# Optimization experiments

Measured on AMD Instinct MI355X. Metric: run time of the kernel, lower is better.

## Reference

```python
import jax, jax.numpy as jnp
import numpy as np

# Grid constants (from init_kwargs)
N_PIX_LO = 256
OVERSAMP = 4
N_PIX_HI = N_PIX_LO * OVERSAMP          # 1024
PIXSCALE_LO = 0.1                        # arcsec / low-res pixel
PIXSCALE_HI = PIXSCALE_LO / OVERSAMP     # arcsec / hi-res pixel
FOV_HALF_HI = 0.5 * (N_PIX_HI - 1) * PIXSCALE_HI
NV = 64
VEL0 = 0.0
DV = 10.0
M = 4_000_000                            # total cloudlet samples (N_clouds * K_vel)

# 8 trilinear corner offsets (x fastest pattern matches torch stacks)
OX = jnp.array([0, 0, 0, 0, 1, 1, 1, 1], dtype=jnp.int32)
OY = jnp.array([0, 0, 1, 1, 0, 0, 1, 1], dtype=jnp.int32)
OV = jnp.array([0, 1, 0, 1, 0, 1, 0, 1], dtype=jnp.int32)


def setup_inputs() -> dict:
    key = jax.random.key(0)
    k1, k2, k3, k4 = jax.random.split(key, 4)
    # positions mostly inside the FoV so most points survive the in-bounds mask
    ra = (jax.random.uniform(k1, (M,), dtype=jnp.float32) - 0.5) * (2.0 * FOV_HALF_HI * 0.95)
    dec = (jax.random.uniform(k2, (M,), dtype=jnp.float32) - 0.5) * (2.0 * FOV_HALF_HI * 0.95)
    vel = jax.random.uniform(k3, (M,), dtype=jnp.float32) * (DV * (NV - 2))
    flux = jax.random.uniform(k4, (M,), dtype=jnp.float32)
    return {"ra": ra, "dec": dec, "vel": vel, "flux": flux}


def _index_and_frac(x):
    i0 = jnp.floor(x)
    return i0.astype(jnp.int32), x - i0


def reference(ra, dec, vel, flux):
    # continuous hi-res grid coordinates
    ix0, fx = _index_and_frac((ra + FOV_HALF_HI) / PIXSCALE_HI)
    iy0, fy = _index_and_frac((dec + FOV_HALF_HI) / PIXSCALE_HI)
    iv0, fv = _index_and_frac((vel - VEL0) / DV)

    # in-bounds mask (instead of boolean compaction, for static shapes under jit)
    mask = ((ix0 >= 0) & (ix0 < N_PIX_HI - 1)
            & (iy0 >= 0) & (iy0 < N_PIX_HI - 1)
            & (iv0 >= 0) & (iv0 < NV - 1))

    # [M, 8] corner indices
    ix = ix0[:, None] + OX
    iy = iy0[:, None] + OY
    iv = iv0[:, None] + OV

    # [M, 8] trilinear weights: (1-f) for offset 0, f for offset 1
    wx = jnp.where(OX == 0, 1.0 - fx[:, None], fx[:, None])
    wy = jnp.where(OY == 0, 1.0 - fy[:, None], fy[:, None])
    wv = jnp.where(OV == 0, 1.0 - fv[:, None], fv[:, None])

    f_w = flux[:, None] * (wx * wy * wv) * mask[:, None].astype(flux.dtype)

    idx = (iv * N_PIX_HI + iy) * N_PIX_HI + ix          # flat voxel index [M, 8]
    idx = jnp.where(mask[:, None], idx, 0)              # out-of-bounds -> bin 0, weight 0

    cube_flat = jnp.zeros(NV * N_PIX_HI * N_PIX_HI, dtype=flux.dtype)
    cube_flat = cube_flat.at[idx.reshape(-1)].add(f_w.reshape(-1))

    # box-downsample: (Nv, H_lo, s, W_lo, s) -> mean over the two oversample axes
    cube_hi = cube_flat.reshape(NV, N_PIX_LO, OVERSAMP, N_PIX_LO, OVERSAMP)
    cube_lo = cube_hi.mean(axis=(-1, -3))               # (Nv, N_pix_lo, N_pix_lo)
    return cube_lo
```

## Files before the change

kernel.cpp:

```cpp
#include <hip/hip_runtime.h>
#include <hip/hip_fp16.h>

constexpr int   kNpixHi = 1024;
constexpr int   kNpixLo = 256;
constexpr int   kNv     = 64;
constexpr float kFov    = 12.7875f;
constexpr float kPsHi   = 0.025f;
constexpr float kDv     = 10.0f;
constexpr float kVel0   = 0.0f;

constexpr int kTileW        = 128;
constexpr int kTileH        = 64;
constexpr int kTilePix      = kTileW * kTileH;
constexpr int kBinsPerPlane = 8;
constexpr int kNumBins      = 64 * kBinsPerPlane;
constexpr int kBinCapIdeal  = 16384;
constexpr int kBinCapMin    = 13500;
constexpr int kThreadsK1    = 512;
constexpr int kWavesK1      = kThreadsK1 / 64;
constexpr int kSamplesPerBlock = 4096;
constexpr int kLdsRecCap    = 8192;
constexpr int kThreadsK2    = 1024;

typedef unsigned int u32x4 __attribute__((ext_vector_type(4)));
typedef unsigned long long u64;

__device__ __forceinline__ u64 pack_rec(unsigned idx, float w0, float w1) {
  const unsigned pk = (unsigned)__half_as_ushort(__float2half(w0))
                    | ((unsigned)__half_as_ushort(__float2half(w1)) << 16);
  return ((u64)pk << 16) | idx;
}

__device__ __forceinline__ void sys_store64(u64* p, u64 v) {
  __hip_atomic_store(p, v, __ATOMIC_RELAXED, __HIP_MEMORY_SCOPE_SYSTEM);
}

__device__ __forceinline__ __half2 h2_from_u32(unsigned pk) {
  return __builtin_bit_cast(__half2, pk);
}

enum EmitMode { kCount, kLds, kDirect };

template <EmitMode MODE>
__device__ __forceinline__ void emit(int bin, unsigned idx, float w0, float w1,
                                     unsigned int* s_cnt,
                                     const unsigned int* s_base,
                                     const unsigned int* s_ofs,
                                     u64* lds_rec,
                                     u64* __restrict__ recs,
                                     unsigned int binCap) {
  if (MODE == kCount) {
    atomicAdd(&s_cnt[bin], 1u);
    return;
  }
  const unsigned off = atomicAdd(&s_cnt[bin], 1u);
  if (MODE == kLds) {
    lds_rec[s_ofs[bin] + off] = pack_rec(idx, w0, w1);
  } else {
    const unsigned slot = s_base[bin] + off;
    if (slot < binCap)
      sys_store64(&recs[(size_t)bin * binCap + slot], pack_rec(idx, w0, w1));
  }
}

template <EmitMode MODE>
__device__ __forceinline__ void process_sample(float rr, float dd, float vv, float ff,
                                               unsigned int* s_cnt,
                                               const unsigned int* s_base,
                                               const unsigned int* s_ofs,
                                               u64* lds_rec,
                                               u64* __restrict__ recs,
                                               unsigned int binCap) {
  const float x = (rr + kFov) / kPsHi;
  const float y = (dd + kFov) / kPsHi;
  const float w = (vv - kVel0) / kDv;

  const float xf = floorf(x), yf = floorf(y), wf = floorf(w);
  const int ix0 = (int)xf, iy0 = (int)yf, iv0 = (int)wf;

  if (ix0 < 0 || ix0 >= kNpixHi - 1 ||
      iy0 < 0 || iy0 >= kNpixHi - 1 ||
      iv0 < 0 || iv0 >= kNv - 1)
    return;

  const float fx = x - xf, fy = y - yf, fv = w - wf;

  const float fw  = ff * 0.0625f;
  const float wv0 = fw * (1.0f - fv);
  const float wv1 = fw * fv;

  const int lx0 = ix0 >> 2, lx1 = (ix0 + 1) >> 2;
  const int ly0 = iy0 >> 2, ly1 = (iy0 + 1) >> 2;
  const bool tx = (lx1 != lx0), ty = (ly1 != ly0);
  const float wx0 = tx ? (1.0f - fx) : 1.0f;
  const float wy0 = ty ? (1.0f - fy) : 1.0f;

#define EMIT_PIX(lx, ly, wxy)                                                \
  {                                                                          \
    const int sb  = (((ly) >> 6) << 1) | ((lx) >> 7);                        \
    const int bin = (iv0 << 3) | sb;                                         \
    const unsigned idx = (unsigned)(((ly) & (kTileH - 1)) * kTileW +         \
                                    ((lx) & (kTileW - 1)));                  \
    emit<MODE>(bin, idx, (wxy) * wv0, (wxy) * wv1,                           \
               s_cnt, s_base, s_ofs, lds_rec, recs, binCap);                 \
  }

  EMIT_PIX(lx0, ly0, wx0 * wy0)
  if (tx)       EMIT_PIX(lx1, ly0, fx * wy0)
  if (ty)       EMIT_PIX(lx0, ly1, wx0 * fy)
  if (tx && ty) EMIT_PIX(lx1, ly1, fx * fy)
#undef EMIT_PIX
}

__global__ __launch_bounds__(kThreadsK1) void scatter_kernel(
    const float* __restrict__ ra, const float* __restrict__ dec,
    const float* __restrict__ vel, const float* __restrict__ flux,
    u64* __restrict__ recs, unsigned int* __restrict__ cursors,
    int m, unsigned int binCap) {
  __shared__ unsigned int s_cnt[kNumBins];
  __shared__ unsigned int s_base[kNumBins];
  __shared__ unsigned int s_ofs[kNumBins];
  __shared__ unsigned int s_wbase[kWavesK1];
  __shared__ unsigned int s_wsum[kWavesK1];
  __shared__ unsigned int s_total;
  __shared__ u64 lds_rec[kLdsRecCap];

  const int tid = threadIdx.x;
  const int blockBase = blockIdx.x * kSamplesPerBlock;
  const int sA = blockBase + tid * 4;
  const int sB = blockBase + kThreadsK1 * 4 + tid * 4;

  float4 rA, dA, vA, fA, rB, dB, vB, fB;

#define LOAD4(s0, r4, d4, v4, f4)                                          \
  if ((s0) + 4 <= m) {                                                     \
    r4 = *reinterpret_cast<const float4*>(ra + (s0));                      \
    d4 = *reinterpret_cast<const float4*>(dec + (s0));                     \
    v4 = *reinterpret_cast<const float4*>(vel + (s0));                     \
    f4 = *reinterpret_cast<const float4*>(flux + (s0));                    \
  } else {                                                                 \
    float* rp = &r4.x; float* dp = &d4.x; float* vp = &v4.x; float* fp = &f4.x; \
    _Pragma("unroll")                                                      \
    for (int k = 0; k < 4; ++k) {                                          \
      const int i = (s0) + k;                                              \
      const bool in = (i < m);                                             \
      rp[k] = in ? ra[i]   : 0.0f;                                         \
      dp[k] = in ? dec[i]  : 0.0f;                                         \
      vp[k] = in ? vel[i]  : -1e9f;                                        \
      fp[k] = in ? flux[i] : 0.0f;                                         \
    }                                                                      \
  }

  LOAD4(sA, rA, dA, vA, fA)
  LOAD4(sB, rB, dB, vB, fB)
#undef LOAD4

  s_cnt[tid] = 0u;
  __syncthreads();

#pragma unroll
  for (int k = 0; k < 4; ++k)
    process_sample<kCount>((&rA.x)[k], (&dA.x)[k], (&vA.x)[k], (&fA.x)[k],
                           s_cnt, s_base, s_ofs, lds_rec, recs, binCap);
#pragma unroll
  for (int k = 0; k < 4; ++k)
    process_sample<kCount>((&rB.x)[k], (&dB.x)[k], (&vB.x)[k], (&fB.x)[k],
                           s_cnt, s_base, s_ofs, lds_rec, recs, binCap);
  __syncthreads();

  const unsigned c = s_cnt[tid];
  unsigned v = c;
#pragma unroll
  for (int d = 1; d < 64; d <<= 1) {
    const unsigned n = __shfl_up(v, d, 64);
    if ((tid & 63) >= d) v += n;
  }
  if ((tid & 63) == 63) s_wsum[tid >> 6] = v;
  __syncthreads();
  if (tid == 0) {
    unsigned acc = 0;
#pragma unroll
    for (int i = 0; i < kWavesK1; ++i) { s_wbase[i] = acc; acc += s_wsum[i]; }
    s_total = acc;
  }
  __syncthreads();
  s_ofs[tid]  = s_wbase[tid >> 6] + v - c;
  s_base[tid] = c ? atomicAdd(&cursors[tid], c) : 0u;
  s_cnt[tid]  = 0u;
  __syncthreads();

  const bool ldsPath = (s_total <= (unsigned)kLdsRecCap);

  if (ldsPath) {
#pragma unroll
    for (int k = 0; k < 4; ++k)
      process_sample<kLds>((&rA.x)[k], (&dA.x)[k], (&vA.x)[k], (&fA.x)[k],
                           s_cnt, s_base, s_ofs, lds_rec, recs, binCap);
#pragma unroll
    for (int k = 0; k < 4; ++k)
      process_sample<kLds>((&rB.x)[k], (&dB.x)[k], (&vB.x)[k], (&fB.x)[k],
                           s_cnt, s_base, s_ofs, lds_rec, recs, binCap);
    __syncthreads();

    const int wave = tid >> 6, lane = tid & 63;
    for (int b = wave; b < kNumBins; b += kWavesK1) {
      const unsigned cnt  = s_cnt[b];
      const unsigned ofs  = s_ofs[b];
      const unsigned base = s_base[b];
      u64* __restrict__ seg = recs + (size_t)b * binCap;
      for (unsigned j = lane; j < cnt; j += 64) {
        const unsigned slot = base + j;
        if (slot < binCap) sys_store64(&seg[slot], lds_rec[ofs + j]);
      }
    }
  } else {
#pragma unroll
    for (int k = 0; k < 4; ++k)
      process_sample<kDirect>((&rA.x)[k], (&dA.x)[k], (&vA.x)[k], (&fA.x)[k],
                              s_cnt, s_base, s_ofs, lds_rec, recs, binCap);
#pragma unroll
    for (int k = 0; k < 4; ++k)
      process_sample<kDirect>((&rB.x)[k], (&dB.x)[k], (&vB.x)[k], (&fB.x)[k],
                              s_cnt, s_base, s_ofs, lds_rec, recs, binCap);
  }
}

__global__ __launch_bounds__(kThreadsK2) void accum_kernel(
    const u64* __restrict__ recs, const unsigned int* __restrict__ cursors,
    unsigned int* __restrict__ tiles, unsigned int binCap) {
  __shared__ __half2 tile2[kTilePix];
  const int bin = blockIdx.x;
  const int tid = threadIdx.x;

  for (int i = tid; i < kTilePix; i += kThreadsK2)
    reinterpret_cast<unsigned*>(tile2)[i] = 0u;
  __syncthreads();

  unsigned cnt = cursors[bin];
  if (cnt > binCap) cnt = binCap;
  const u64* __restrict__ rb = recs + (size_t)bin * binCap;
  const u32x4* __restrict__ rb4 = reinterpret_cast<const u32x4*>(rb);

  const unsigned npair = cnt >> 1;
  for (unsigned j = (unsigned)tid; j < npair; j += kThreadsK2) {
    const u32x4 q = rb4[j];
    const unsigned idx0 = q.x & 0xFFFFu;
    const unsigned pk0  = (q.x >> 16) | (q.y << 16);
    unsafeAtomicAdd(&tile2[idx0], h2_from_u32(pk0));
    const unsigned idx1 = q.z & 0xFFFFu;
    const unsigned pk1  = (q.z >> 16) | (q.w << 16);
    unsafeAtomicAdd(&tile2[idx1], h2_from_u32(pk1));
  }
  if ((cnt & 1u) && tid == 0) {
    const u64 r = rb[cnt - 1];
    unsafeAtomicAdd(&tile2[(unsigned)r & 0xFFFFu],
                    h2_from_u32((unsigned)(r >> 16)));
  }
  __syncthreads();

  unsigned int* __restrict__ dst = tiles + (size_t)bin * kTilePix;
  const unsigned* __restrict__ src = reinterpret_cast<const unsigned*>(tile2);
  for (int g = tid; g < kTilePix / 4; g += kThreadsK2) {
    *reinterpret_cast<u32x4*>(dst + g * 4) =
        *reinterpret_cast<const u32x4*>(src + g * 4);
  }
}

__global__ __launch_bounds__(256) void convert_kernel(
    const unsigned int* __restrict__ tiles, float* __restrict__ out) {
  const int t   = blockIdx.x * blockDim.x + threadIdx.x;
  const int bin = t >> 11;
  const int g   = t & 2047;
  const int idx = g * 4;

  const u32x4 cur = *reinterpret_cast<const u32x4*>(
      tiles + (size_t)bin * kTilePix + idx);
  const int v = bin >> 3;
  u32x4 prv = {0u, 0u, 0u, 0u};
  if (v > 0)
    prv = *reinterpret_cast<const u32x4*>(
        tiles + (size_t)(bin - kBinsPerPlane) * kTilePix + idx);

  float4 r;
#pragma unroll
  for (int k = 0; k < 4; ++k) {
    const __half2 c = h2_from_u32(cur[k]);
    const __half2 p = h2_from_u32(prv[k]);
    (&r.x)[k] = __low2float(c) + ((v > 0) ? __high2float(p) : 0.0f);
  }

  const int sb = bin & 7;
  const int ry = idx >> 7, rx = idx & (kTileW - 1);
  const size_t o = (size_t)v * (kNpixLo * kNpixLo)
                 + (size_t)((sb >> 1) * kTileH + ry) * kNpixLo
                 + (size_t)(sb & 1) * kTileW + rx;
  *reinterpret_cast<float4*>(out + o) = r;
}

__device__ __forceinline__ void splat2(float* __restrict__ out, int planeBase,
                                       int lx, int ly, float wxy,
                                       float wv0, float wv1) {
  const int s = ly * kNpixLo + lx;
  atomicAdd(out + planeBase + s, wxy * wv0);
  atomicAdd(out + planeBase + kNpixLo * kNpixLo + s, wxy * wv1);
}

__global__ __launch_bounds__(256) void cloud_raster_direct(
    const float* __restrict__ ra, const float* __restrict__ dec,
    const float* __restrict__ vel, const float* __restrict__ flux,
    float* __restrict__ out, int m) {
  const int t    = blockIdx.x * blockDim.x + threadIdx.x;
  const int base = t * 4;
  if (base >= m) return;
  float4 r4, d4, v4, f4;
  if (base + 4 <= m) {
    r4 = *reinterpret_cast<const float4*>(ra + base);
    d4 = *reinterpret_cast<const float4*>(dec + base);
    v4 = *reinterpret_cast<const float4*>(vel + base);
    f4 = *reinterpret_cast<const float4*>(flux + base);
  } else {
    float* rp = &r4.x; float* dp = &d4.x; float* vp = &v4.x; float* fp = &f4.x;
#pragma unroll
    for (int k = 0; k < 4; ++k) {
      const int i = base + k;
      rp[k] = (i < m) ? ra[i]   : 0.0f;
      dp[k] = (i < m) ? dec[i]  : 0.0f;
      vp[k] = (i < m) ? vel[i]  : -1e9f;
      fp[k] = (i < m) ? flux[i] : 0.0f;
    }
  }
#pragma unroll
  for (int k = 0; k < 4; ++k) {
    const float rr = (&r4.x)[k], dd = (&d4.x)[k], vv = (&v4.x)[k], ff = (&f4.x)[k];
    const float x = (rr + kFov) / kPsHi;
    const float y = (dd + kFov) / kPsHi;
    const float w = (vv - kVel0) / kDv;
    const float xf = floorf(x), yf = floorf(y), wf = floorf(w);
    const int ix0 = (int)xf, iy0 = (int)yf, iv0 = (int)wf;
    if (ix0 < 0 || ix0 >= kNpixHi - 1 || iy0 < 0 || iy0 >= kNpixHi - 1 ||
        iv0 < 0 || iv0 >= kNv - 1)
      continue;
    const float fx = x - xf, fy = y - yf, fv = w - wf;
    const float fw  = ff * 0.0625f;
    const float wv0 = fw * (1.0f - fv);
    const float wv1 = fw * fv;
    const int lx0 = ix0 >> 2, lx1 = (ix0 + 1) >> 2;
    const int ly0 = iy0 >> 2, ly1 = (iy0 + 1) >> 2;
    const bool tx = (lx1 != lx0), ty = (ly1 != ly0);
    const float wx0 = tx ? (1.0f - fx) : 1.0f;
    const float wy0 = ty ? (1.0f - fy) : 1.0f;
    const int pb = iv0 * (kNpixLo * kNpixLo);
    splat2(out, pb, lx0, ly0, wx0 * wy0, wv0, wv1);
    if (tx)       splat2(out, pb, lx1, ly0, fx  * wy0, wv0, wv1);
    if (ty)       splat2(out, pb, lx0, ly1, wx0 * fy,  wv0, wv1);
    if (tx && ty) splat2(out, pb, lx1, ly1, fx  * fy,  wv0, wv1);
  }
}


extern "C" void kernel_launch(void* const* d_in, const int* in_sizes, int n_in,
                              void* d_out, int out_size, void* d_ws, size_t ws_size,
                              hipStream_t stream) {
  (void)n_in;
  const float* ra   = (const float*)d_in[0];
  const float* dec  = (const float*)d_in[1];
  const float* vel  = (const float*)d_in[2];
  const float* flux = (const float*)d_in[3];
  float* out = (float*)d_out;
  const int m = in_sizes[0];

  constexpr size_t kCursorBytes = 4096;
  constexpr size_t kTileBytes   = (size_t)kNumBins * kTilePix * 4;
  unsigned int binCap = 0;
  if (ws_size > kCursorBytes + kTileBytes) {
    const size_t avail = (ws_size - kCursorBytes - kTileBytes) / ((size_t)kNumBins * 8);
    binCap = (unsigned int)(avail < (size_t)kBinCapIdeal ? avail : (size_t)kBinCapIdeal);
    binCap &= ~1u;
  }

  if (binCap >= kBinCapMin) {
    unsigned int* cursors = (unsigned int*)d_ws;
    unsigned int* tiles   = (unsigned int*)((char*)d_ws + kCursorBytes);
    u64* recs = (u64*)((char*)d_ws + kCursorBytes + kTileBytes);
    hipError_t e = hipMemsetAsync(d_ws, 0, kCursorBytes, stream); (void)e;
    const int blocks = (m + kSamplesPerBlock - 1) / kSamplesPerBlock;
    scatter_kernel<<<blocks, kThreadsK1, 0, stream>>>(ra, dec, vel, flux, recs, cursors, m, binCap);
    accum_kernel<<<kNumBins, kThreadsK2, 0, stream>>>(recs, cursors, tiles, binCap);
    convert_kernel<<<(kNumBins * (kTilePix / 4)) / 256, 256, 0, stream>>>(tiles, out);
  } else {
    hipError_t e = hipMemsetAsync(d_out, 0, (size_t)out_size * sizeof(float), stream); (void)e;
    const int threads = 256;
    const int nThreads = (m + 3) / 4;
    const int blocks = (nThreads + threads - 1) / threads;
    cloud_raster_direct<<<blocks, threads, 0, stream>>>(ra, dec, vel, flux, out, m);
  }
}
```

Baseline: 107.7 us.

## Replace two-pass count/scan binning with single-pass fixed LDS slices plus overflow

Drops the counting pass, the block-wide prefix scan and its barriers. Each sample is now binned once into fixed per-bin LDS slices of 18 records. Records past a slice go to a small register stash or straight to global memory through per-record global atomics on the bin cursor. This removes recomputing every sample and several syncthreads, at the cost of global atomics for overflow records and a lot of LDS (512×18×8 bytes), which may lower occupancy.

```diff
diff --git a/kernel.cpp b/kernel.cpp
--- a/kernel.cpp
+++ b/kernel.cpp
@@ -19,7 +19,7 @@
 constexpr int kThreadsK1    = 512;
 constexpr int kWavesK1      = kThreadsK1 / 64;
 constexpr int kSamplesPerBlock = 4096;
-constexpr int kLdsRecCap    = 8192;
+constexpr int kSlice        = 18;
 constexpr int kThreadsK2    = 1024;
 
 typedef unsigned int u32x4 __attribute__((ext_vector_type(4)));
@@ -39,38 +39,38 @@
   return __builtin_bit_cast(__half2, pk);
 }
 
-enum EmitMode { kCount, kLds, kDirect };
-
-template <EmitMode MODE>
-__device__ __forceinline__ void emit(int bin, unsigned idx, float w0, float w1,
-                                     unsigned int* s_cnt,
-                                     const unsigned int* s_base,
-                                     const unsigned int* s_ofs,
-                                     u64* lds_rec,
-                                     u64* __restrict__ recs,
-                                     unsigned int binCap) {
-  if (MODE == kCount) {
-    atomicAdd(&s_cnt[bin], 1u);
-    return;
-  }
+struct Stash {
+  unsigned bin0, bin1, bin2, bin3;
+  u64 rec0, rec1, rec2, rec3;
+  int n;
+};
+
+__device__ __forceinline__ void emit_rec(int bin, unsigned idx, float w0, float w1,
+                                         unsigned int* s_cnt, u64* lds_rec,
+                                         unsigned int* __restrict__ cursors,
+                                         u64* __restrict__ recs,
+                                         unsigned int binCap, Stash& st) {
+  const u64 rec = pack_rec(idx, w0, w1);
   const unsigned off = atomicAdd(&s_cnt[bin], 1u);
-  if (MODE == kLds) {
-    lds_rec[s_ofs[bin] + off] = pack_rec(idx, w0, w1);
+  if (off < (unsigned)kSlice) {
+    lds_rec[bin * kSlice + off] = rec;
+  } else if (st.n < 4) {
+    if      (st.n == 0) { st.bin0 = bin; st.rec0 = rec; }
+    else if (st.n == 1) { st.bin1 = bin; st.rec1 = rec; }
+    else if (st.n == 2) { st.bin2 = bin; st.rec2 = rec; }
+    else                { st.bin3 = bin; st.rec3 = rec; }
+    st.n++;
   } else {
-    const unsigned slot = s_base[bin] + off;
-    if (slot < binCap)
-      sys_store64(&recs[(size_t)bin * binCap + slot], pack_rec(idx, w0, w1));
-  }
-}
-
-template <EmitMode MODE>
+    const unsigned slot = atomicAdd(&cursors[bin], 1u);
+    if (slot < binCap) sys_store64(&recs[(size_t)bin * binCap + slot], rec);
+  }
+}
+
 __device__ __forceinline__ void process_sample(float rr, float dd, float vv, float ff,
-                                               unsigned int* s_cnt,
-                                               const unsigned int* s_base,
-                                               const unsigned int* s_ofs,
-                                               u64* lds_rec,
+                                               unsigned int* s_cnt, u64* lds_rec,
+                                               unsigned int* __restrict__ cursors,
                                                u64* __restrict__ recs,
-                                               unsigned int binCap) {
+                                               unsigned int binCap, Stash& st) {
   const float x = (rr + kFov) / kPsHi;
   const float y = (dd + kFov) / kPsHi;
   const float w = (vv - kVel0) / kDv;
@@ -101,8 +101,8 @@
     const int bin = (iv0 << 3) | sb;                                         \
     const unsigned idx = (unsigned)(((ly) & (kTileH - 1)) * kTileW +         \
                                     ((lx) & (kTileW - 1)));                  \
-    emit<MODE>(bin, idx, (wxy) * wv0, (wxy) * wv1,                           \
-               s_cnt, s_base, s_ofs, lds_rec, recs, binCap);                 \
+    emit_rec(bin, idx, (wxy) * wv0, (wxy) * wv1,                             \
+             s_cnt, lds_rec, cursors, recs, binCap, st);                     \
   }
 
   EMIT_PIX(lx0, ly0, wx0 * wy0)
@@ -119,11 +119,7 @@
     int m, unsigned int binCap) {
   __shared__ unsigned int s_cnt[kNumBins];
   __shared__ unsigned int s_base[kNumBins];
-  __shared__ unsigned int s_ofs[kNumBins];
-  __shared__ unsigned int s_wbase[kWavesK1];
-  __shared__ unsigned int s_wsum[kWavesK1];
-  __shared__ unsigned int s_total;
-  __shared__ u64 lds_rec[kLdsRecCap];
+  __shared__ u64 lds_rec[kNumBins * kSlice];
 
   const int tid = threadIdx.x;
   const int blockBase = blockIdx.x * kSamplesPerBlock;
@@ -158,70 +154,55 @@
   s_cnt[tid] = 0u;
   __syncthreads();
 
+  Stash st;
+  st.n = 0;
+  st.bin0 = st.bin1 = st.bin2 = st.bin3 = 0u;
+  st.rec0 = st.rec1 = st.rec2 = st.rec3 = 0ull;
+
 #pragma unroll
   for (int k = 0; k < 4; ++k)
-    process_sample<kCount>((&rA.x)[k], (&dA.x)[k], (&vA.x)[k], (&fA.x)[k],
-                           s_cnt, s_base, s_ofs, lds_rec, recs, binCap);
+    process_sample((&rA.x)[k], (&dA.x)[k], (&vA.x)[k], (&fA.x)[k],
+                   s_cnt, lds_rec, cursors, recs, binCap, st);
 #pragma unroll
   for (int k = 0; k < 4; ++k)
-    process_sample<kCount>((&rB.x)[k], (&dB.x)[k], (&vB.x)[k], (&fB.x)[k],
-                           s_cnt, s_base, s_ofs, lds_rec, recs, binCap);
-  __syncthreads();
-
-  const unsigned c = s_cnt[tid];
-  unsigned v = c;
-#pragma unroll
-  for (int d = 1; d < 64; d <<= 1) {
-    const unsigned n = __shfl_up(v, d, 64);
-    if ((tid & 63) >= d) v += n;
-  }
-  if ((tid & 63) == 63) s_wsum[tid >> 6] = v;
-  __syncthreads();
-  if (tid == 0) {
-    unsigned acc = 0;
-#pragma unroll
-    for (int i = 0; i < kWavesK1; ++i) { s_wbase[i] = acc; acc += s_wsum[i]; }
-    s_total = acc;
-  }
-  __syncthreads();
-  s_ofs[tid]  = s_wbase[tid >> 6] + v - c;
-  s_base[tid] = c ? atomicAdd(&cursors[tid], c) : 0u;
-  s_cnt[tid]  = 0u;
-  __syncthreads();
-
-  const bool ldsPath = (s_total <= (unsigned)kLdsRecCap);
-
-  if (ldsPath) {
-#pragma unroll
-    for (int k = 0; k < 4; ++k)
-      process_sample<kLds>((&rA.x)[k], (&dA.x)[k], (&vA.x)[k], (&fA.x)[k],
-                           s_cnt, s_base, s_ofs, lds_rec, recs, binCap);
-#pragma unroll
-    for (int k = 0; k < 4; ++k)
-      process_sample<kLds>((&rB.x)[k], (&dB.x)[k], (&vB.x)[k], (&fB.x)[k],
-                           s_cnt, s_base, s_ofs, lds_rec, recs, binCap);
-    __syncthreads();
-
-    const int wave = tid >> 6, lane = tid & 63;
-    for (int b = wave; b < kNumBins; b += kWavesK1) {
-      const unsigned cnt  = s_cnt[b];
-      const unsigned ofs  = s_ofs[b];
-      const unsigned base = s_base[b];
-      u64* __restrict__ seg = recs + (size_t)b * binCap;
-      for (unsigned j = lane; j < cnt; j += 64) {
-        const unsigned slot = base + j;
-        if (slot < binCap) sys_store64(&seg[slot], lds_rec[ofs + j]);
-      }
+    process_sample((&rB.x)[k], (&dB.x)[k], (&vB.x)[k], (&fB.x)[k],
+                   s_cnt, lds_rec, cursors, recs, binCap, st);
+
+  if (st.n > 0) {
+    const unsigned slot = atomicAdd(&cursors[st.bin0], 1u);
+    if (slot < binCap) sys_store64(&recs[(size_t)st.bin0 * binCap + slot], st.rec0);
+  }
+  if (st.n > 1) {
+    const unsigned slot = atomicAdd(&cursors[st.bin1], 1u);
+    if (slot < binCap) sys_store64(&recs[(size_t)st.bin1 * binCap + slot], st.rec1);
+  }
+  if (st.n > 2) {
+    const unsigned slot = atomicAdd(&cursors[st.bin2], 1u);
+    if (slot < binCap) sys_store64(&recs[(size_t)st.bin2 * binCap + slot], st.rec2);
+  }
+  if (st.n > 3) {
+    const unsigned slot = atomicAdd(&cursors[st.bin3], 1u);
+    if (slot < binCap) sys_store64(&recs[(size_t)st.bin3 * binCap + slot], st.rec3);
+  }
+  __syncthreads();
+
+  {
+    const unsigned c0 = s_cnt[tid];
+    const unsigned c  = c0 < (unsigned)kSlice ? c0 : (unsigned)kSlice;
+    s_base[tid] = c ? atomicAdd(&cursors[tid], c) : 0u;
+    s_cnt[tid]  = c;
+  }
+  __syncthreads();
+
+  const int wave = tid >> 6, lane = tid & 63;
+  for (int b = wave; b < kNumBins; b += kWavesK1) {
+    const unsigned cnt  = s_cnt[b];
+    const unsigned base = s_base[b];
+    u64* __restrict__ seg = recs + (size_t)b * binCap;
+    for (unsigned j = lane; j < cnt; j += 64) {
+      const unsigned slot = base + j;
+      if (slot < binCap) sys_store64(&seg[slot], lds_rec[b * kSlice + j]);
     }
-  } else {
-#pragma unroll
-    for (int k = 0; k < 4; ++k)
-      process_sample<kDirect>((&rA.x)[k], (&dA.x)[k], (&vA.x)[k], (&fA.x)[k],
-                              s_cnt, s_base, s_ofs, lds_rec, recs, binCap);
-#pragma unroll
-    for (int k = 0; k < 4; ++k)
-      process_sample<kDirect>((&rB.x)[k], (&dB.x)[k], (&vB.x)[k], (&fB.x)[k],
-                              s_cnt, s_base, s_ofs, lds_rec, recs, binCap);
   }
 }
 
```

New measurement: 224.2 us. 108% more time.
